# Performance work log

Hardware: AMD Instinct MI355X
Metric: run time of the kernel (lower is better)

## Reference

```python
import jax, jax.numpy as jnp
import numpy as np

K_CONST = 1.0  # margin constant K from __init__


def setup_inputs() -> dict:
    key = jax.random.key(0)
    k1, k2, k3 = jax.random.split(key, 3)
    m, n, d = 2048, 100000, 128
    return {
        "X_tilde": jax.random.normal(k1, (m, d), dtype=jnp.float32),
        "X": jax.random.normal(k2, (n, d), dtype=jnp.float32),
        "w": jax.random.normal(k3, (n, 1), dtype=jnp.float32),
        "k": 10,
    }


def reference(X_tilde, X, w, k):
    # w_prime = sqrt((max(w) - w) / K), appended as extra coordinate for the
    # augmented exact L2 search (queries padded with 0 in that coordinate).
    w_prime2 = (jnp.max(w) - w)[:, 0] / K_CONST  # (n,) == w_prime**2
    # squared L2 in augmented space: ||q||^2 + ||x||^2 + w_prime^2 - 2 q.x
    q2 = jnp.sum(X_tilde * X_tilde, axis=1, keepdims=True)           # (m,1)
    x2 = jnp.sum(X * X, axis=1) + w_prime2                            # (n,)
    d2 = q2 + x2[None, :] - 2.0 * (X_tilde @ X.T)                     # (m,n)
    _, idx = jax.lax.top_k(-d2, k)                                    # (m,k) nearest
    # gather neighbors and recompute actual (non-augmented) L2 distance
    nb = X[idx]                                                       # (m,k,d)
    diff = nb - X_tilde[:, None, :]
    dist = jnp.sqrt(jnp.sum(diff * diff, axis=2))                     # (m,k)
    act = w[idx, 0] - K_CONST * dist                                  # (m,k)
    # argmax + gather == max over the k neighbors
    return jnp.max(act, axis=1)                                       # (m,)
```

## Files before the change

### kernel.cpp

```cpp
#include <hip/hip_runtime.h>
#include <math.h>

typedef __attribute__((ext_vector_type(8))) short short8;
typedef __attribute__((ext_vector_type(16))) float f32x16;

#define D      128
#define NSEG   128
#define SEGC   800
#define NT     25
#define TILE_C 32
#define KTOP   10
#define CAP    128
#define DELTA  3.0f
#define NPAD   (NSEG * SEGC + TILE_C)
#define ROWU   144
#define TUNITS (TILE_C * 18)
#define BUFU   (TUNITS * 8)

__device__ __forceinline__ int lds_unit(int u) {
    int r = u / 18, kb = u % 18;
    return r * 18 + (kb ^ ((r >> 2) & 1));
}

__device__ __forceinline__ ushort f2bf(float f) {
    uint u = __float_as_uint(f);
    uint r = (u + 0x7FFFu + ((u >> 16) & 1u)) >> 16;
    return (ushort)r;
}

__device__ __forceinline__ uint packx2(float x2w) {
    ushort h = f2bf(x2w);
    float hf = __uint_as_float(((uint)h) << 16);
    ushort lo = f2bf(x2w - hf);
    return (uint)h | ((uint)lo << 16);
}

__device__ __forceinline__ void insert10(float s, float v, float ls[KTOP], float lw[KTOP]) {
    ls[9] = s; lw[9] = v;
#pragma unroll
    for (int p = 9; p > 0; --p) {
        bool sw = ls[p] < ls[p - 1];
        float ts = sw ? ls[p - 1] : ls[p];
        float tl = sw ? ls[p]     : ls[p - 1];
        float tv = sw ? lw[p - 1] : lw[p];
        float tu = sw ? lw[p]     : lw[p - 1];
        ls[p] = ts; ls[p - 1] = tl;
        lw[p] = tv; lw[p - 1] = tu;
    }
}

__device__ __forceinline__ void insert10s(float s, float ms[KTOP]) {
    ms[9] = s;
#pragma unroll
    for (int p = 9; p > 0; --p) {
        float a = fminf(ms[p - 1], ms[p]);
        float b = fmaxf(ms[p - 1], ms[p]);
        ms[p - 1] = a; ms[p] = b;
    }
}

__global__ void prep_kernel(const float* __restrict__ Xt, const float* __restrict__ X,
                            const float* __restrict__ w,
                            ushort* __restrict__ Xbp, ushort* __restrict__ Xtb,
                            float* __restrict__ x2wf, float* __restrict__ q2f,
                            int* __restrict__ cnt, int n, int m, int nblocksA) {
    int wave = threadIdx.x >> 6, lane = threadIdx.x & 63;
    if ((int)blockIdx.x < nblocksA) {
        int row = blockIdx.x * 4 + wave;
        if (row >= NPAD) return;
        ushort* rowp = Xbp + (size_t)row * ROWU;
        if (row < n) {
            float2 v = ((const float2*)X)[(size_t)row * 64 + lane];
            ((ushort2*)rowp)[lane] = make_ushort2(f2bf(v.x), f2bf(v.y));
            float s = v.x * v.x + v.y * v.y;
#pragma unroll
            for (int o = 32; o; o >>= 1) s += __shfl_xor(s, o, 64);
            float x2w = s - w[row];
            if (lane == 0) x2wf[row] = x2w;
            if (lane < 8) ((uint*)rowp)[64 + lane] = (lane == 0) ? packx2(x2w) : 0u;
        } else {
            ((ushort2*)rowp)[lane] = make_ushort2(0, 0);
            if (lane < 8) ((uint*)rowp)[64 + lane] = (lane == 0) ? packx2(1e30f) : 0u;
        }
    } else {
        int qb = blockIdx.x - nblocksA;
        int row = qb * 4 + wave;
        int tid = qb * 256 + threadIdx.x;
        if (tid < m) cnt[tid] = 0;
        if (row >= m) return;
        float2 v = ((const float2*)Xt)[(size_t)row * 64 + lane];
        ((ushort2*)Xtb)[(size_t)row * 64 + lane] = make_ushort2(f2bf(v.x), f2bf(v.y));
        float s = v.x * v.x + v.y * v.y;
#pragma unroll
        for (int o = 32; o; o >>= 1) s += __shfl_xor(s, o, 64);
        if (lane == 0) q2f[row] = s;
    }
}

__device__ __forceinline__ void emit_cand(int q, int c, int* cnt, int* buf) {
    int pos = atomicAdd(&cnt[q], 1);
    if (pos < CAP) buf[q * CAP + pos] = c;
}

template<int PASS>
__global__ __launch_bounds__(256, 2) void nd_pass(
        const ushort* __restrict__ Xbp, const ushort* __restrict__ Xtb,
        const float* __restrict__ tau, float* __restrict__ minbuf,
        int* __restrict__ cnt, int* __restrict__ buf, int m) {
    __shared__ __align__(16) ushort As[2 * BUFU];

    const int t = threadIdx.x;
    const int l = t & 63, wv = t >> 6;
    const int half = l >> 5;
    const int seg = blockIdx.x;
    const int qbase = blockIdx.y * 512 + wv * 128;
    const int q0 = qbase + (l & 31);
    const int tile0 = seg * NT;
    const int halfx = half ^ ((l >> 2) & 1);

    short8 Bf[9][4];
#pragma unroll
    for (int s = 0; s < 8; ++s)
#pragma unroll
        for (int qs = 0; qs < 4; ++qs)
            Bf[s][qs] = *(const short8*)(Xtb + (size_t)(q0 + qs * 32) * D + s * 16 + half * 8);
    {
        short8 z = (short8)(short)0;
        if (l < 32) { z[0] = (short)0xBF00; z[1] = (short)0xBF00; }
#pragma unroll
        for (int qs = 0; qs < 4; ++qs) Bf[8][qs] = z;
    }

    float tp[4];
    float mx[4];
#pragma unroll
    for (int qs = 0; qs < 4; ++qs) {
        tp[qs] = (PASS == 2) ? (-0.5f * tau[q0 + qs * 32]) : 0.f;
        mx[qs] = -INFINITY;
    }

    const int u0 = t, u1 = 256 + t, u2 = 512 + (t & 63);
    const int L0 = lds_unit(u0) * 8, L1 = lds_unit(u1) * 8, L2 = lds_unit(u2) * 8;
    const uint4* Xg = (const uint4*)Xbp;

    uint4 r0 = Xg[(size_t)tile0 * TUNITS + u0];
    uint4 r1 = Xg[(size_t)tile0 * TUNITS + u1];
    uint4 r2 = make_uint4(0, 0, 0, 0);
    if (t < 64) r2 = Xg[(size_t)tile0 * TUNITS + u2];

    for (int t2 = 0; t2 < NT; ++t2) {
        ushort* Lb = &As[(t2 & 1) * BUFU];
        *(uint4*)&Lb[L0] = r0;
        *(uint4*)&Lb[L1] = r1;
        if (t < 64) *(uint4*)&Lb[L2] = r2;
        __syncthreads();

        const size_t gb = (size_t)(tile0 + t2 + 1) * TUNITS;
        r0 = Xg[gb + u0];
        r1 = Xg[gb + u1];
        if (t < 64) r2 = Xg[gb + u2];

        f32x16 acc0 = (f32x16)0.f, acc1 = (f32x16)0.f, acc2 = (f32x16)0.f, acc3 = (f32x16)0.f;
#pragma unroll
        for (int ks = 0; ks < 9; ++ks) {
            const int kb = (ks < 8) ? (ks * 2 + halfx) : (16 + halfx);
            short8 a = *(const short8*)&Lb[((l & 31) * 18 + kb) * 8];
            acc0 = __builtin_amdgcn_mfma_f32_32x32x16_bf16(a, Bf[ks][0], acc0, 0, 0, 0);
            acc1 = __builtin_amdgcn_mfma_f32_32x32x16_bf16(a, Bf[ks][1], acc1, 0, 0, 0);
            acc2 = __builtin_amdgcn_mfma_f32_32x32x16_bf16(a, Bf[ks][2], acc2, 0, 0, 0);
            acc3 = __builtin_amdgcn_mfma_f32_32x32x16_bf16(a, Bf[ks][3], acc3, 0, 0, 0);
        }

        float h[4];
#pragma unroll
        for (int qs = 0; qs < 4; ++qs) h[qs] = -INFINITY;
#pragma unroll
        for (int r = 0; r < 16; ++r) {
            h[0] = fmaxf(h[0], acc0[r]); h[1] = fmaxf(h[1], acc1[r]);
            h[2] = fmaxf(h[2], acc2[r]); h[3] = fmaxf(h[3], acc3[r]);
        }
        if (PASS == 1) {
#pragma unroll
            for (int qs = 0; qs < 4; ++qs) mx[qs] = fmaxf(mx[qs], h[qs]);
        } else {
            const int base = (tile0 + t2) * TILE_C;
            if (__any(h[0] >= tp[0])) {
#pragma unroll
                for (int r = 0; r < 16; ++r)
                    if (acc0[r] >= tp[0]) emit_cand(q0,      base + (r & 3) + 8 * (r >> 2) + 4 * half, cnt, buf);
            }
            if (__any(h[1] >= tp[1])) {
#pragma unroll
                for (int r = 0; r < 16; ++r)
                    if (acc1[r] >= tp[1]) emit_cand(q0 + 32, base + (r & 3) + 8 * (r >> 2) + 4 * half, cnt, buf);
            }
            if (__any(h[2] >= tp[2])) {
#pragma unroll
                for (int r = 0; r < 16; ++r)
                    if (acc2[r] >= tp[2]) emit_cand(q0 + 64, base + (r & 3) + 8 * (r >> 2) + 4 * half, cnt, buf);
            }
            if (__any(h[3] >= tp[3])) {
#pragma unroll
                for (int r = 0; r < 16; ++r)
                    if (acc3[r] >= tp[3]) emit_cand(q0 + 96, base + (r & 3) + 8 * (r >> 2) + 4 * half, cnt, buf);
            }
        }
    }

    if (PASS == 1) {
        size_t rowi = (size_t)(seg * 2 + half) * m;
#pragma unroll
        for (int qs = 0; qs < 4; ++qs)
            minbuf[rowi + q0 + qs * 32] = -2.f * mx[qs];
    }
}

__global__ void tau_kernel(const float* __restrict__ minbuf, float* __restrict__ tau, int m) {
    __shared__ float sh[64 * 40];
    const int qi = threadIdx.x & 63, part = threadIdx.x >> 6;
    const int q = blockIdx.x * 64 + qi;
    float ms[KTOP];
#pragma unroll
    for (int e = 0; e < KTOP; ++e) ms[e] = INFINITY;
#pragma unroll 4
    for (int i = 0; i < 64; ++i) {
        float v = minbuf[(size_t)(part * 64 + i) * m + q];
        if (v < ms[9]) insert10s(v, ms);
    }
#pragma unroll
    for (int e = 0; e < KTOP; ++e) sh[qi * 40 + part * 10 + e] = ms[e];
    __syncthreads();
    if (threadIdx.x < 64) {
        const int qq = blockIdx.x * 64 + threadIdx.x;
        float fs[KTOP];
#pragma unroll
        for (int e = 0; e < KTOP; ++e) fs[e] = INFINITY;
        for (int x = 0; x < 40; ++x) {
            float v = sh[threadIdx.x * 40 + x];
            if (v < fs[9]) insert10s(v, fs);
        }
        tau[qq] = fs[9] + DELTA;
    }
}

__global__ void rescore_kernel(const float* __restrict__ Xtf, const float* __restrict__ Xf,
                               const float* __restrict__ w, const float* __restrict__ x2wf,
                               const float* __restrict__ q2f, const int* __restrict__ cnt,
                               const int* __restrict__ buf, float* __restrict__ out, int m) {
    __shared__ float sS[CAP], sW[CAP];
    const int q = blockIdx.x, l = threadIdx.x;
    const int c = min(cnt[q], CAP);
    const bool v0 = l < c, v1 = l + 64 < c;
    const int j0 = v0 ? buf[q * CAP + l] : 0;
    const int j1 = v1 ? buf[q * CAP + l + 64] : 0;
    const float4* Q4 = (const float4*)Xtf + (size_t)q * 32;
    const float4* A4 = (const float4*)Xf + (size_t)j0 * 32;
    const float4* B4 = (const float4*)Xf + (size_t)j1 * 32;
    float acc0 = 0.f, acc1 = 0.f;
#pragma unroll 8
    for (int d = 0; d < 32; ++d) {
        float4 qv = Q4[d];
        float4 a = A4[d], b = B4[d];
        acc0 = fmaf(qv.x, a.x, fmaf(qv.y, a.y, fmaf(qv.z, a.z, fmaf(qv.w, a.w, acc0))));
        acc1 = fmaf(qv.x, b.x, fmaf(qv.y, b.y, fmaf(qv.z, b.z, fmaf(qv.w, b.w, acc1))));
    }
    sS[l]      = v0 ? (x2wf[j0] - 2.f * acc0) : INFINITY;
    sW[l]      = v0 ? w[j0] : 0.f;
    sS[l + 64] = v1 ? (x2wf[j1] - 2.f * acc1) : INFINITY;
    sW[l + 64] = v1 ? w[j1] : 0.f;
    __syncthreads();
    if (l == 0) {
        float ls[KTOP], lw[KTOP];
#pragma unroll
        for (int e = 0; e < KTOP; ++e) { ls[e] = INFINITY; lw[e] = 0.f; }
        for (int i = 0; i < c; ++i)
            if (sS[i] < ls[9]) insert10(sS[i], sW[i], ls, lw);
        float q2v = q2f[q];
        float mxv = -INFINITY;
#pragma unroll
        for (int e = 0; e < KTOP; ++e) {
            if (ls[e] < 1e30f) {
                float d2 = fmaxf(q2v + ls[e] + lw[e], 0.f);
                mxv = fmaxf(mxv, lw[e] - sqrtf(d2));
            }
        }
        out[q] = mxv;
    }
}

extern "C" void kernel_launch(void* const* d_in, const int* in_sizes, int n_in,
                              void* d_out, int out_size, void* d_ws, size_t ws_size,
                              hipStream_t stream) {
    const float* Xt = (const float*)d_in[0];
    const float* X  = (const float*)d_in[1];
    const float* w  = (const float*)d_in[2];
    const int m = in_sizes[0] / D;
    const int n = in_sizes[1] / D;

    auto align256 = [](size_t x) { return (x + 255) & ~(size_t)255; };
    char* p = (char*)d_ws;
    ushort* Xbp  = (ushort*)p;  p += align256((size_t)NPAD * ROWU * 2);
    ushort* Xtb  = (ushort*)p;  p += align256((size_t)m * D * 2);
    float*  x2wf = (float*)p;   p += align256((size_t)n * 4);
    float*  q2f  = (float*)p;   p += align256((size_t)m * 4);
    float*  minb = (float*)p;   p += align256((size_t)2 * NSEG * m * 4);
    float*  tau  = (float*)p;   p += align256((size_t)m * 4);
    int*    cnt  = (int*)p;     p += align256((size_t)m * 4);
    int*    buf  = (int*)p;     p += align256((size_t)m * CAP * 4);

    const int nblocksA = (NPAD + 3) / 4;
    const int nblocksB = (m + 3) / 4;
    prep_kernel<<<nblocksA + nblocksB, 256, 0, stream>>>(Xt, X, w, Xbp, Xtb, x2wf, q2f, cnt, n, m, nblocksA);

    dim3 grid(NSEG, m / 512);
    nd_pass<1><<<grid, 256, 0, stream>>>(Xbp, Xtb, tau, minb, cnt, buf, m);
    tau_kernel<<<m / 64, 256, 0, stream>>>(minb, tau, m);
    nd_pass<2><<<grid, 256, 0, stream>>>(Xbp, Xtb, tau, minb, cnt, buf, m);
    rescore_kernel<<<m, 64, 0, stream>>>(Xt, X, w, x2wf, q2f, cnt, buf, (float*)d_out, m);
}
```

Baseline: 267.4 us.

## Halve per-wave query tile to raise occupancy in distance passes

Each wave now covers 64 queries (two 32-query MFMA subtiles) instead of 128, so each block covers 256 queries, the grid's y-dimension doubles, and launch bounds rise from 2 to 4 blocks per SIMD. Register pressure drops because fewer B fragments and accumulators are held. The aim is more waves in flight to hide memory and LDS latency. In exchange, every X tile is loaded from global memory and staged through LDS twice as often, which lowers reuse of each A fragment across queries.

```diff
diff --git a/kernel.cpp b/kernel.cpp
--- a/kernel.cpp
+++ b/kernel.cpp
@@ -103,7 +103,7 @@
 }
 
 template<int PASS>
-__global__ __launch_bounds__(256, 2) void nd_pass(
+__global__ __launch_bounds__(256, 4) void nd_pass(
         const ushort* __restrict__ Xbp, const ushort* __restrict__ Xtb,
         const float* __restrict__ tau, float* __restrict__ minbuf,
         int* __restrict__ cnt, int* __restrict__ buf, int m) {
@@ -113,28 +113,24 @@
     const int l = t & 63, wv = t >> 6;
     const int half = l >> 5;
     const int seg = blockIdx.x;
-    const int qbase = blockIdx.y * 512 + wv * 128;
+    const int qbase = blockIdx.y * 256 + wv * 64;
     const int q0 = qbase + (l & 31);
     const int tile0 = seg * NT;
     const int halfx = half ^ ((l >> 2) & 1);
 
-    short8 Bf[9][4];
+    short8 Bf[8][2];
 #pragma unroll
     for (int s = 0; s < 8; ++s)
 #pragma unroll
-        for (int qs = 0; qs < 4; ++qs)
+        for (int qs = 0; qs < 2; ++qs)
             Bf[s][qs] = *(const short8*)(Xtb + (size_t)(q0 + qs * 32) * D + s * 16 + half * 8);
-    {
-        short8 z = (short8)(short)0;
-        if (l < 32) { z[0] = (short)0xBF00; z[1] = (short)0xBF00; }
-#pragma unroll
-        for (int qs = 0; qs < 4; ++qs) Bf[8][qs] = z;
-    }
-
-    float tp[4];
-    float mx[4];
-#pragma unroll
-    for (int qs = 0; qs < 4; ++qs) {
+    short8 B8 = (short8)(short)0;
+    if (l < 32) { B8[0] = (short)0xBF00; B8[1] = (short)0xBF00; }
+
+    float tp[2];
+    float mx[2];
+#pragma unroll
+    for (int qs = 0; qs < 2; ++qs) {
         tp[qs] = (PASS == 2) ? (-0.5f * tau[q0 + qs * 32]) : 0.f;
         mx[qs] = -INFINITY;
     }
@@ -160,28 +156,26 @@
         r1 = Xg[gb + u1];
         if (t < 64) r2 = Xg[gb + u2];
 
-        f32x16 acc0 = (f32x16)0.f, acc1 = (f32x16)0.f, acc2 = (f32x16)0.f, acc3 = (f32x16)0.f;
+        f32x16 acc0 = (f32x16)0.f, acc1 = (f32x16)0.f;
 #pragma unroll
         for (int ks = 0; ks < 9; ++ks) {
             const int kb = (ks < 8) ? (ks * 2 + halfx) : (16 + halfx);
             short8 a = *(const short8*)&Lb[((l & 31) * 18 + kb) * 8];
-            acc0 = __builtin_amdgcn_mfma_f32_32x32x16_bf16(a, Bf[ks][0], acc0, 0, 0, 0);
-            acc1 = __builtin_amdgcn_mfma_f32_32x32x16_bf16(a, Bf[ks][1], acc1, 0, 0, 0);
-            acc2 = __builtin_amdgcn_mfma_f32_32x32x16_bf16(a, Bf[ks][2], acc2, 0, 0, 0);
-            acc3 = __builtin_amdgcn_mfma_f32_32x32x16_bf16(a, Bf[ks][3], acc3, 0, 0, 0);
-        }
-
-        float h[4];
-#pragma unroll
-        for (int qs = 0; qs < 4; ++qs) h[qs] = -INFINITY;
+            short8 b0 = (ks < 8) ? Bf[ks][0] : B8;
+            short8 b1 = (ks < 8) ? Bf[ks][1] : B8;
+            acc0 = __builtin_amdgcn_mfma_f32_32x32x16_bf16(a, b0, acc0, 0, 0, 0);
+            acc1 = __builtin_amdgcn_mfma_f32_32x32x16_bf16(a, b1, acc1, 0, 0, 0);
+        }
+
+        float h[2];
+        h[0] = -INFINITY; h[1] = -INFINITY;
 #pragma unroll
         for (int r = 0; r < 16; ++r) {
             h[0] = fmaxf(h[0], acc0[r]); h[1] = fmaxf(h[1], acc1[r]);
-            h[2] = fmaxf(h[2], acc2[r]); h[3] = fmaxf(h[3], acc3[r]);
         }
         if (PASS == 1) {
-#pragma unroll
-            for (int qs = 0; qs < 4; ++qs) mx[qs] = fmaxf(mx[qs], h[qs]);
+            mx[0] = fmaxf(mx[0], h[0]);
+            mx[1] = fmaxf(mx[1], h[1]);
         } else {
             const int base = (tile0 + t2) * TILE_C;
             if (__any(h[0] >= tp[0])) {
@@ -194,24 +188,13 @@
                 for (int r = 0; r < 16; ++r)
                     if (acc1[r] >= tp[1]) emit_cand(q0 + 32, base + (r & 3) + 8 * (r >> 2) + 4 * half, cnt, buf);
             }
-            if (__any(h[2] >= tp[2])) {
-#pragma unroll
-                for (int r = 0; r < 16; ++r)
-                    if (acc2[r] >= tp[2]) emit_cand(q0 + 64, base + (r & 3) + 8 * (r >> 2) + 4 * half, cnt, buf);
-            }
-            if (__any(h[3] >= tp[3])) {
-#pragma unroll
-                for (int r = 0; r < 16; ++r)
-                    if (acc3[r] >= tp[3]) emit_cand(q0 + 96, base + (r & 3) + 8 * (r >> 2) + 4 * half, cnt, buf);
-            }
         }
     }
 
     if (PASS == 1) {
         size_t rowi = (size_t)(seg * 2 + half) * m;
-#pragma unroll
-        for (int qs = 0; qs < 4; ++qs)
-            minbuf[rowi + q0 + qs * 32] = -2.f * mx[qs];
+        minbuf[rowi + q0]      = -2.f * mx[0];
+        minbuf[rowi + q0 + 32] = -2.f * mx[1];
     }
 }
 
@@ -312,7 +295,7 @@
     const int nblocksB = (m + 3) / 4;
     prep_kernel<<<nblocksA + nblocksB, 256, 0, stream>>>(Xt, X, w, Xbp, Xtb, x2wf, q2f, cnt, n, m, nblocksA);
 
-    dim3 grid(NSEG, m / 512);
+    dim3 grid(NSEG, m / 256);
     nd_pass<1><<<grid, 256, 0, stream>>>(Xbp, Xtb, tau, minb, cnt, buf, m);
     tau_kernel<<<m / 64, 256, 0, stream>>>(minb, tau, m);
     nd_pass<2><<<grid, 256, 0, stream>>>(Xbp, Xtb, tau, minb, cnt, buf, m);
```

Measured after the change: 273.1 us. 1.02x slower.
